# Kernel tuning notes

Hardware: AMD Instinct MI355X
Metric: run time of the kernel (lower is better)

## Reference

```python
import jax, jax.numpy as jnp
import numpy as np

N_NODES = 100000
N_EDGES = 800000
D_MODEL = 128
N_HEAD = 8
LN_EPS = 1e-6


def setup_inputs() -> dict:
    key = jax.random.key(0)
    ks = jax.random.split(key, 6)
    embeds = jax.random.normal(ks[0], (N_NODES, D_MODEL), dtype=jnp.float32)
    # xavier_uniform bound for square [d, d] matrix: sqrt(6 / (d + d))
    bound = float(np.sqrt(6.0 / (D_MODEL + D_MODEL)))
    qW = jax.random.uniform(ks[1], (D_MODEL, D_MODEL), minval=-bound, maxval=bound, dtype=jnp.float32)
    kW = jax.random.uniform(ks[2], (D_MODEL, D_MODEL), minval=-bound, maxval=bound, dtype=jnp.float32)
    vW = jax.random.uniform(ks[3], (D_MODEL, D_MODEL), minval=-bound, maxval=bound, dtype=jnp.float32)
    ln_gamma = jnp.ones((D_MODEL,), dtype=jnp.float32)
    ln_beta = jnp.zeros((D_MODEL,), dtype=jnp.float32)
    edge_index = jax.random.randint(ks[4], (2, N_EDGES), 0, N_NODES, dtype=jnp.int64)
    return {"embeds": embeds, "qW": qW, "kW": kW, "vW": vW,
            "ln_gamma": ln_gamma, "ln_beta": ln_beta, "edge_index": edge_index}


def reference(embeds, qW, kW, vW, ln_gamma, ln_beta, edge_index):
    rows = edge_index[0]  # destination (softmax segment) indices, [E]
    cols = edge_index[1]  # source indices, [E]
    n_nodes, d_model = embeds.shape
    n_edges = rows.shape[0]
    head = N_HEAD
    d_head = d_model // head

    row_e = embeds[rows]                      # [E, d]
    col_e = embeds[cols]                      # [E, d]
    q = (row_e @ qW).reshape(n_edges, head, d_head)
    k = (col_e @ kW).reshape(n_edges, head, d_head)
    v = (col_e @ vW).reshape(n_edges, head, d_head)

    att = jnp.einsum('ehd,ehd->eh', q, k)     # [E, h]
    att = jnp.clip(att, -10.0, 10.0)
    exp_att = jnp.exp(att)

    # segment-softmax normalization over destination node
    att_norm = jax.ops.segment_sum(exp_att, rows, num_segments=n_nodes)  # [N, h]
    att = exp_att / (att_norm[rows] + 1e-8)   # [E, h]

    res_e = (att[:, :, None] * v).reshape(n_edges, d_model)              # [E, d]
    res = jax.ops.segment_sum(res_e, rows, num_segments=n_nodes)         # [N, d]
    res = res + embeds

    # LayerNorm(eps=1e-6) over last dim
    mean = jnp.mean(res, axis=-1, keepdims=True)
    var = jnp.mean((res - mean) ** 2, axis=-1, keepdims=True)
    out = (res - mean) * jax.lax.rsqrt(var + LN_EPS) * ln_gamma + ln_beta
    return out
```

## Files before the change

kernel.cpp:

```cpp
#include <hip/hip_runtime.h>
#include <hip/hip_bf16.h>

#define N_NODES 100000
#define N_EDGES 800000
#define D 128
#define NH 8
#define NB ((N_NODES + 255) / 256)

typedef __hip_bfloat16 bf16;
typedef __bf16 bf16x8 __attribute__((ext_vector_type(8)));
typedef float  f32x4  __attribute__((ext_vector_type(4)));

__device__ __forceinline__ unsigned short f2bu(float x) {
    bf16 b = __float2bfloat16(x);
    return *reinterpret_cast<unsigned short*>(&b);
}
__device__ __forceinline__ float bu2f(unsigned short u) {
    return __uint_as_float(((unsigned)u) << 16);
}
__device__ __forceinline__ float bfe0(unsigned u) { return __uint_as_float(u << 16); }
__device__ __forceinline__ float bfe1(unsigned u) { return __uint_as_float(u & 0xffff0000u); }

union frag_u { unsigned short u[8]; bf16x8 v; };

__global__ __launch_bounds__(256) void wf_prep(
    const float* __restrict__ Wq, const float* __restrict__ Wk, const float* __restrict__ Wv,
    unsigned short* __restrict__ Wf)
{
    int t = blockIdx.x * 256 + threadIdx.x;
    if (t >= 3 * 32 * 64) return;
    int lane = t & 63;
    int ct   = (t >> 6) & 31;
    int mat  = t >> 11;
    const float* W = (mat == 0) ? Wq : (mat == 1) ? Wk : Wv;
    int c  = ct >> 3, tt = ct & 7;
    int n  = tt * 16 + (lane & 15);
    int kb = c * 32 + (lane >> 4) * 8;
    unsigned short* dst = Wf + (size_t)mat * 32768 + (size_t)ct * 1024 + (size_t)lane * 8;
#pragma unroll
    for (int j = 0; j < 8; ++j) {
        float w  = W[(size_t)(kb + j) * D + n];
        unsigned short hb = f2bu(w);
        float lo = w - bu2f(hb);
        dst[j]       = hb;
        dst[512 + j] = f2bu(lo);
    }
}

__global__ __launch_bounds__(256) void qkv_mfma(
    const float* __restrict__ E, const unsigned short* __restrict__ Wf,
    bf16* __restrict__ Q, bf16* __restrict__ K, bf16* __restrict__ V)
{
    __shared__ unsigned short bsh[16384];
    const int tid  = threadIdx.x;
    const int wave = tid >> 6;
    const int lane = tid & 63;
    const int r0w  = blockIdx.x * 128 + wave * 32;

    const int am = lane & 15;
    const int aq = lane >> 4;

    frag_u ahi[2][4], alo[2][4];
#pragma unroll
    for (int rt = 0; rt < 2; ++rt) {
        int row = r0w + rt * 16 + am;
        if (row >= N_NODES) row = N_NODES - 1;
        const float* erow = E + (size_t)row * D + aq * 8;
#pragma unroll
        for (int c = 0; c < 4; ++c) {
            float4 e0 = *reinterpret_cast<const float4*>(erow + c * 32);
            float4 e1 = *reinterpret_cast<const float4*>(erow + c * 32 + 4);
            float ef[8] = {e0.x, e0.y, e0.z, e0.w, e1.x, e1.y, e1.z, e1.w};
#pragma unroll
            for (int j = 0; j < 8; ++j) {
                unsigned short hb = f2bu(ef[j]);
                ahi[rt][c].u[j] = hb;
                alo[rt][c].u[j] = f2bu(ef[j] - bu2f(hb));
            }
        }
    }

    bf16* const Os[3] = {Q, K, V};

#pragma unroll
    for (int mat = 0; mat < 3; ++mat) {
        f32x4 acc[8][2];
#pragma unroll
        for (int t = 0; t < 8; ++t)
#pragma unroll
            for (int rt = 0; rt < 2; ++rt)
                acc[t][rt] = (f32x4){0.f, 0.f, 0.f, 0.f};

        const unsigned short* wm = Wf + (size_t)mat * 32768;

#pragma unroll
        for (int half = 0; half < 2; ++half) {
            __syncthreads();
            const uint4* src = reinterpret_cast<const uint4*>(wm + half * 16384);
            uint4* dstv = reinterpret_cast<uint4*>(bsh);
#pragma unroll
            for (int k = 0; k < 8; ++k)
                dstv[k * 256 + tid] = src[k * 256 + tid];
            __syncthreads();

#pragma unroll
            for (int t = 0; t < 8; ++t) {
#pragma unroll
                for (int cc = 0; cc < 2; ++cc) {
                    const unsigned short* bp = bsh + (cc * 8 + t) * 1024 + lane * 8;
                    bf16x8 bhi = *reinterpret_cast<const bf16x8*>(bp);
                    bf16x8 blo = *reinterpret_cast<const bf16x8*>(bp + 512);
                    const int c = half * 2 + cc;
#pragma unroll
                    for (int rt = 0; rt < 2; ++rt) {
                        acc[t][rt] = __builtin_amdgcn_mfma_f32_16x16x32_bf16(alo[rt][c].v, bhi, acc[t][rt], 0, 0, 0);
                        acc[t][rt] = __builtin_amdgcn_mfma_f32_16x16x32_bf16(ahi[rt][c].v, blo, acc[t][rt], 0, 0, 0);
                        acc[t][rt] = __builtin_amdgcn_mfma_f32_16x16x32_bf16(ahi[rt][c].v, bhi, acc[t][rt], 0, 0, 0);
                    }
                }
            }
        }
        __syncthreads();

        unsigned short* ob = bsh + wave * 2176;
#pragma unroll
        for (int rt = 0; rt < 2; ++rt) {
#pragma unroll
            for (int t = 0; t < 8; ++t)
#pragma unroll
                for (int r = 0; r < 4; ++r)
                    ob[(aq * 4 + r) * 136 + t * 16 + am] = f2bu(acc[t][rt][r]);
            const int row = lane >> 2, c4 = lane & 3;
            int grow = r0w + rt * 16 + row;
            if (grow < N_NODES) {
                const uint4* srcb = reinterpret_cast<const uint4*>(ob + row * 136 + c4 * 32);
                uint4 d0 = srcb[0], d1 = srcb[1], d2 = srcb[2], d3 = srcb[3];
                uint4* dst = reinterpret_cast<uint4*>(Os[mat] + (size_t)grow * D + c4 * 32);
                dst[0] = d0; dst[1] = d1; dst[2] = d2; dst[3] = d3;
            }
        }
    }
}

__global__ __launch_bounds__(256) void hist_kernel(
    const int* __restrict__ rows, int* __restrict__ counts)
{
    int e = blockIdx.x * 256 + threadIdx.x;
    if (e < N_EDGES) atomicAdd(&counts[rows[e]], 1);
}

__global__ __launch_bounds__(256) void scan_block(
    const int* __restrict__ counts, int* __restrict__ scanned, int* __restrict__ block_sums)
{
    __shared__ int s[256];
    int tid = threadIdx.x;
    int i = blockIdx.x * 256 + tid;
    int v = (i < N_NODES) ? counts[i] : 0;
    s[tid] = v;
    __syncthreads();
#pragma unroll
    for (int off = 1; off < 256; off <<= 1) {
        int t = (tid >= off) ? s[tid - off] : 0;
        __syncthreads();
        s[tid] += t;
        __syncthreads();
    }
    if (i < N_NODES) scanned[i] = s[tid] - v;
    if (tid == 255) block_sums[blockIdx.x] = s[255];
}

__global__ __launch_bounds__(512) void scan_tops(int* __restrict__ block_sums)
{
    __shared__ int s[512];
    int tid = threadIdx.x;
    int v = (tid < NB) ? block_sums[tid] : 0;
    s[tid] = v;
    __syncthreads();
#pragma unroll
    for (int off = 1; off < 512; off <<= 1) {
        int t = (tid >= off) ? s[tid - off] : 0;
        __syncthreads();
        s[tid] += t;
        __syncthreads();
    }
    if (tid < NB) block_sums[tid] = s[tid] - v;
}

__global__ __launch_bounds__(256) void scan_add(
    int* __restrict__ scanned, const int* __restrict__ block_sums, int* __restrict__ cursor)
{
    int i = blockIdx.x * 256 + threadIdx.x;
    if (i < N_NODES) {
        int o = scanned[i] + block_sums[blockIdx.x];
        scanned[i] = o;
        cursor[i]  = o;
    }
}

__global__ __launch_bounds__(256) void scatter_kernel(
    const int* __restrict__ rows, const int* __restrict__ cols,
    int* __restrict__ cursor, int* __restrict__ csr_cols)
{
    int e = blockIdx.x * 256 + threadIdx.x;
    if (e < N_EDGES) {
        int pos = atomicAdd(&cursor[rows[e]], 1);
        csr_cols[pos] = cols[e];
    }
}

__global__ __launch_bounds__(256) void fused_node(
    const bf16* __restrict__ Qb, const bf16* __restrict__ Kb, const bf16* __restrict__ Vb,
    const int* __restrict__ offsets, const int* __restrict__ counts,
    const int* __restrict__ csr_cols,
    const float* __restrict__ emb,
    const float* __restrict__ gamma, const float* __restrict__ beta,
    float* __restrict__ out)
{
    int n = blockIdx.x * 4 + (threadIdx.x >> 6);
    int lane = threadIdx.x & 63;
    if (n >= N_NODES) return;

    unsigned qu = *reinterpret_cast<const unsigned*>(Qb + (size_t)n * D + lane * 2);
    float q0 = bfe0(qu), q1 = bfe1(qu);

    int start = offsets[n];
    int cnt   = counts[n];

    const bf16* kbase = Kb + lane * 2;
    const bf16* vbase = Vb + lane * 2;

    float acc0 = 0.f, acc1 = 0.f, nrm = 0.f;
    for (int base = 0; base < cnt; base += 64) {
        int m = cnt - base; if (m > 64) m = 64;
        int myc = (base + lane < cnt) ? csr_cols[start + base + lane] : 0;
        int j = 0;
        for (; j + 1 < m; j += 2) {
            int c0 = __shfl(myc, j, 64);
            int c1 = __shfl(myc, j + 1, 64);
            unsigned ku0 = *reinterpret_cast<const unsigned*>(kbase + (size_t)c0 * D);
            unsigned vu0 = *reinterpret_cast<const unsigned*>(vbase + (size_t)c0 * D);
            unsigned ku1 = *reinterpret_cast<const unsigned*>(kbase + (size_t)c1 * D);
            unsigned vu1 = *reinterpret_cast<const unsigned*>(vbase + (size_t)c1 * D);
            float p0 = q0 * bfe0(ku0) + q1 * bfe1(ku0);
            float p1 = q0 * bfe0(ku1) + q1 * bfe1(ku1);
            p0 += __shfl_xor(p0, 1, 64);
            p1 += __shfl_xor(p1, 1, 64);
            p0 += __shfl_xor(p0, 2, 64);
            p1 += __shfl_xor(p1, 2, 64);
            p0 += __shfl_xor(p0, 4, 64);
            p1 += __shfl_xor(p1, 4, 64);
            float s0 = __expf(fminf(fmaxf(p0, -10.f), 10.f));
            float s1 = __expf(fminf(fmaxf(p1, -10.f), 10.f));
            nrm  += s0 + s1;
            acc0 += s0 * bfe0(vu0) + s1 * bfe0(vu1);
            acc1 += s0 * bfe1(vu0) + s1 * bfe1(vu1);
        }
        if (j < m) {
            int c0 = __shfl(myc, j, 64);
            unsigned ku0 = *reinterpret_cast<const unsigned*>(kbase + (size_t)c0 * D);
            unsigned vu0 = *reinterpret_cast<const unsigned*>(vbase + (size_t)c0 * D);
            float p0 = q0 * bfe0(ku0) + q1 * bfe1(ku0);
            p0 += __shfl_xor(p0, 1, 64);
            p0 += __shfl_xor(p0, 2, 64);
            p0 += __shfl_xor(p0, 4, 64);
            float s0 = __expf(fminf(fmaxf(p0, -10.f), 10.f));
            nrm  += s0;
            acc0 += s0 * bfe0(vu0);
            acc1 += s0 * bfe1(vu0);
        }
    }

    float w = 1.f / (nrm + 1e-8f);
    float2 e2 = *reinterpret_cast<const float2*>(emb + (size_t)n * D + lane * 2);
    float x0 = acc0 * w + e2.x;
    float x1 = acc1 * w + e2.y;

    float ssum = x0 + x1;
#pragma unroll
    for (int off = 32; off; off >>= 1) ssum += __shfl_xor(ssum, off, 64);
    float mean = ssum * (1.0f / 128.0f);
    float d0 = x0 - mean, d1 = x1 - mean;
    float var = d0 * d0 + d1 * d1;
#pragma unroll
    for (int off = 32; off; off >>= 1) var += __shfl_xor(var, off, 64);
    float rs = rsqrtf(var * (1.0f / 128.0f) + 1e-6f);

    float2 g2 = *reinterpret_cast<const float2*>(gamma + lane * 2);
    float2 b2 = *reinterpret_cast<const float2*>(beta + lane * 2);
    float2 o2 = make_float2(d0 * rs * g2.x + b2.x, d1 * rs * g2.y + b2.y);
    *reinterpret_cast<float2*>(out + (size_t)n * D + lane * 2) = o2;
}

extern "C" void kernel_launch(void* const* d_in, const int* in_sizes, int n_in,
                              void* d_out, int out_size, void* d_ws, size_t ws_size,
                              hipStream_t stream)
{
    const float* emb   = (const float*)d_in[0];
    const float* qW    = (const float*)d_in[1];
    const float* kW    = (const float*)d_in[2];
    const float* vW    = (const float*)d_in[3];
    const float* gamma = (const float*)d_in[4];
    const float* beta  = (const float*)d_in[5];
    const int*   eidx  = (const int*)d_in[6];
    const int*   rows  = eidx;
    const int*   cols  = eidx + N_EDGES;
    float* out = (float*)d_out;

    const size_t ND = (size_t)N_NODES * D;
    bf16* Qb = (bf16*)d_ws;
    bf16* Kb = Qb + ND;
    bf16* Vb = Kb + ND;
    int* counts     = (int*)(Vb + ND);
    int* offsets    = counts + N_NODES;
    int* cursor     = offsets + N_NODES;
    int* block_sums = cursor + N_NODES;
    int* csr_cols   = block_sums + 512;
    unsigned short* Wf = (unsigned short*)(csr_cols + N_EDGES);

    hipMemsetAsync(counts, 0, (size_t)N_NODES * sizeof(int), stream);

    wf_prep<<<24, 256, 0, stream>>>(qW, kW, vW, Wf);
    qkv_mfma<<<(N_NODES + 127) / 128, 256, 0, stream>>>(emb, Wf, Qb, Kb, Vb);

    hist_kernel<<<(N_EDGES + 255) / 256, 256, 0, stream>>>(rows, counts);
    scan_block<<<NB, 256, 0, stream>>>(counts, offsets, block_sums);
    scan_tops<<<1, 512, 0, stream>>>(block_sums);
    scan_add<<<NB, 256, 0, stream>>>(offsets, block_sums, cursor);
    scatter_kernel<<<(N_EDGES + 255) / 256, 256, 0, stream>>>(rows, cols, cursor, csr_cols);

    fused_node<<<(N_NODES + 3) / 4, 256, 0, stream>>>(
        Qb, Kb, Vb, offsets, counts, csr_cols, emb, gamma, beta, out);
}
```

Baseline: 315.3 us.

## Interleave K/V per node and process eight edges per wave with per-lane head slices

K and V projections are written into one interleaved [N,256] buffer so each gathered neighbor's K and V sit in one contiguous 512-byte row. The aggregation kernel now assigns each lane a (head, edge-slot) pair, so a wave handles eight edges at once, with each lane loading 32-byte K and V slices and computing a full head dot product locally instead of using shuffle reductions. Partial sums across slots are combined with a shuffle reduction at the end. This trades per-edge shuffles and narrow 4-byte gathers for wider loads and more registers (16 accumulators plus K/V floats), and wastes lanes when a node has a degree not divisible by eight.

```diff
diff --git a/kernel.cpp b/kernel.cpp
--- a/kernel.cpp
+++ b/kernel.cpp
@@ -20,6 +20,13 @@
 }
 __device__ __forceinline__ float bfe0(unsigned u) { return __uint_as_float(u << 16); }
 __device__ __forceinline__ float bfe1(unsigned u) { return __uint_as_float(u & 0xffff0000u); }
+
+__device__ __forceinline__ void ext8(uint4 u, float* f) {
+    f[0] = bfe0(u.x); f[1] = bfe1(u.x);
+    f[2] = bfe0(u.y); f[3] = bfe1(u.y);
+    f[4] = bfe0(u.z); f[5] = bfe1(u.z);
+    f[6] = bfe0(u.w); f[7] = bfe1(u.w);
+}
 
 union frag_u { unsigned short u[8]; bf16x8 v; };
 
@@ -49,7 +56,7 @@
 
 __global__ __launch_bounds__(256) void qkv_mfma(
     const float* __restrict__ E, const unsigned short* __restrict__ Wf,
-    bf16* __restrict__ Q, bf16* __restrict__ K, bf16* __restrict__ V)
+    bf16* __restrict__ Q, bf16* __restrict__ KV)
 {
     __shared__ unsigned short bsh[16384];
     const int tid  = threadIdx.x;
@@ -79,8 +86,6 @@
             }
         }
     }
-
-    bf16* const Os[3] = {Q, K, V};
 
 #pragma unroll
     for (int mat = 0; mat < 3; ++mat) {
@@ -135,7 +140,10 @@
             if (grow < N_NODES) {
                 const uint4* srcb = reinterpret_cast<const uint4*>(ob + row * 136 + c4 * 32);
                 uint4 d0 = srcb[0], d1 = srcb[1], d2 = srcb[2], d3 = srcb[3];
-                uint4* dst = reinterpret_cast<uint4*>(Os[mat] + (size_t)grow * D + c4 * 32);
+                bf16* base = (mat == 0)
+                    ? (Q  + (size_t)grow * D)
+                    : (KV + (size_t)grow * 256 + (mat == 1 ? 0 : 128));
+                uint4* dst = reinterpret_cast<uint4*>(base + c4 * 32);
                 dst[0] = d0; dst[1] = d1; dst[2] = d2; dst[3] = d3;
             }
         }
@@ -209,7 +217,7 @@
 }
 
 __global__ __launch_bounds__(256) void fused_node(
-    const bf16* __restrict__ Qb, const bf16* __restrict__ Kb, const bf16* __restrict__ Vb,
+    const bf16* __restrict__ Qb, const bf16* __restrict__ KV,
     const int* __restrict__ offsets, const int* __restrict__ counts,
     const int* __restrict__ csr_cols,
     const float* __restrict__ emb,
@@ -219,61 +227,62 @@
     int n = blockIdx.x * 4 + (threadIdx.x >> 6);
     int lane = threadIdx.x & 63;
     if (n >= N_NODES) return;
-
-    unsigned qu = *reinterpret_cast<const unsigned*>(Qb + (size_t)n * D + lane * 2);
-    float q0 = bfe0(qu), q1 = bfe1(qu);
+    const int head = lane & 7;
+    const int slot = lane >> 3;
+
+    const uint4* qp = reinterpret_cast<const uint4*>(Qb + (size_t)n * D + head * 16);
+    uint4 qa = qp[0], qb_ = qp[1];
+    float qf[16];
+    ext8(qa, qf); ext8(qb_, qf + 8);
 
     int start = offsets[n];
     int cnt   = counts[n];
 
-    const bf16* kbase = Kb + lane * 2;
-    const bf16* vbase = Vb + lane * 2;
-
-    float acc0 = 0.f, acc1 = 0.f, nrm = 0.f;
+    float acc[16];
+#pragma unroll
+    for (int i = 0; i < 16; ++i) acc[i] = 0.f;
+    float nrm = 0.f;
+
     for (int base = 0; base < cnt; base += 64) {
         int m = cnt - base; if (m > 64) m = 64;
         int myc = (base + lane < cnt) ? csr_cols[start + base + lane] : 0;
-        int j = 0;
-        for (; j + 1 < m; j += 2) {
-            int c0 = __shfl(myc, j, 64);
-            int c1 = __shfl(myc, j + 1, 64);
-            unsigned ku0 = *reinterpret_cast<const unsigned*>(kbase + (size_t)c0 * D);
-            unsigned vu0 = *reinterpret_cast<const unsigned*>(vbase + (size_t)c0 * D);
-            unsigned ku1 = *reinterpret_cast<const unsigned*>(kbase + (size_t)c1 * D);
-            unsigned vu1 = *reinterpret_cast<const unsigned*>(vbase + (size_t)c1 * D);
-            float p0 = q0 * bfe0(ku0) + q1 * bfe1(ku0);
-            float p1 = q0 * bfe0(ku1) + q1 * bfe1(ku1);
-            p0 += __shfl_xor(p0, 1, 64);
-            p1 += __shfl_xor(p1, 1, 64);
-            p0 += __shfl_xor(p0, 2, 64);
-            p1 += __shfl_xor(p1, 2, 64);
-            p0 += __shfl_xor(p0, 4, 64);
-            p1 += __shfl_xor(p1, 4, 64);
-            float s0 = __expf(fminf(fmaxf(p0, -10.f), 10.f));
-            float s1 = __expf(fminf(fmaxf(p1, -10.f), 10.f));
-            nrm  += s0 + s1;
-            acc0 += s0 * bfe0(vu0) + s1 * bfe0(vu1);
-            acc1 += s0 * bfe1(vu0) + s1 * bfe1(vu1);
+        for (int g = 0; g < m; g += 8) {
+            int j = g + slot;
+            int c = __shfl(myc, j, 64);
+            const uint4* kvp = reinterpret_cast<const uint4*>(KV + (size_t)c * 256 + head * 16);
+            uint4 k0 = kvp[0], k1 = kvp[1];
+            uint4 v0 = kvp[16], v1 = kvp[17];
+            float kf[16], vf[16];
+            ext8(k0, kf); ext8(k1, kf + 8);
+            float p = 0.f;
+#pragma unroll
+            for (int i = 0; i < 16; ++i) p += qf[i] * kf[i];
+            float s = __expf(fminf(fmaxf(p, -10.f), 10.f));
+            if (j >= m) s = 0.f;
+            nrm += s;
+            ext8(v0, vf); ext8(v1, vf + 8);
+#pragma unroll
+            for (int i = 0; i < 16; ++i) acc[i] += s * vf[i];
         }
-        if (j < m) {
-            int c0 = __shfl(myc, j, 64);
-            unsigned ku0 = *reinterpret_cast<const unsigned*>(kbase + (size_t)c0 * D);
-            unsigned vu0 = *reinterpret_cast<const unsigned*>(vbase + (size_t)c0 * D);
-            float p0 = q0 * bfe0(ku0) + q1 * bfe1(ku0);
-            p0 += __shfl_xor(p0, 1, 64);
-            p0 += __shfl_xor(p0, 2, 64);
-            p0 += __shfl_xor(p0, 4, 64);
-            float s0 = __expf(fminf(fmaxf(p0, -10.f), 10.f));
-            nrm  += s0;
-            acc0 += s0 * bfe0(vu0);
-            acc1 += s0 * bfe1(vu0);
-        }
+    }
+
+#pragma unroll
+    for (int off = 8; off <= 32; off <<= 1) {
+        nrm += __shfl_xor(nrm, off, 64);
+#pragma unroll
+        for (int i = 0; i < 16; ++i) acc[i] += __shfl_xor(acc[i], off, 64);
     }
 
     float w = 1.f / (nrm + 1e-8f);
-    float2 e2 = *reinterpret_cast<const float2*>(emb + (size_t)n * D + lane * 2);
-    float x0 = acc0 * w + e2.x;
-    float x1 = acc1 * w + e2.y;
+    float a0 = 0.f, a1 = 0.f;
+#pragma unroll
+    for (int s2 = 0; s2 < 8; ++s2)
+        if (slot == s2) { a0 = acc[2 * s2]; a1 = acc[2 * s2 + 1]; }
+
+    int di = head * 16 + slot * 2;
+    float2 e2 = *reinterpret_cast<const float2*>(emb + (size_t)n * D + di);
+    float x0 = a0 * w + e2.x;
+    float x1 = a1 * w + e2.y;
 
     float ssum = x0 + x1;
 #pragma unroll
@@ -285,10 +294,10 @@
     for (int off = 32; off; off >>= 1) var += __shfl_xor(var, off, 64);
     float rs = rsqrtf(var * (1.0f / 128.0f) + 1e-6f);
 
-    float2 g2 = *reinterpret_cast<const float2*>(gamma + lane * 2);
-    float2 b2 = *reinterpret_cast<const float2*>(beta + lane * 2);
+    float2 g2 = *reinterpret_cast<const float2*>(gamma + di);
+    float2 b2 = *reinterpret_cast<const float2*>(beta + di);
     float2 o2 = make_float2(d0 * rs * g2.x + b2.x, d1 * rs * g2.y + b2.y);
-    *reinterpret_cast<float2*>(out + (size_t)n * D + lane * 2) = o2;
+    *reinterpret_cast<float2*>(out + (size_t)n * D + di) = o2;
 }
 
 extern "C" void kernel_launch(void* const* d_in, const int* in_sizes, int n_in,
@@ -308,9 +317,8 @@
 
     const size_t ND = (size_t)N_NODES * D;
     bf16* Qb = (bf16*)d_ws;
-    bf16* Kb = Qb + ND;
-    bf16* Vb = Kb + ND;
-    int* counts     = (int*)(Vb + ND);
+    bf16* KV = Qb + ND;
+    int* counts     = (int*)(KV + 2 * ND);
     int* offsets    = counts + N_NODES;
     int* cursor     = offsets + N_NODES;
     int* block_sums = cursor + N_NODES;
@@ -320,7 +328,7 @@
     hipMemsetAsync(counts, 0, (size_t)N_NODES * sizeof(int), stream);
 
     wf_prep<<<24, 256, 0, stream>>>(qW, kW, vW, Wf);
-    qkv_mfma<<<(N_NODES + 127) / 128, 256, 0, stream>>>(emb, Wf, Qb, Kb, Vb);
+    qkv_mfma<<<(N_NODES + 127) / 128, 256, 0, stream>>>(emb, Wf, Qb, KV);
 
     hist_kernel<<<(N_EDGES + 255) / 256, 256, 0, stream>>>(rows, counts);
     scan_block<<<NB, 256, 0, stream>>>(counts, offsets, block_sums);
@@ -329,5 +337,5 @@
     scatter_kernel<<<(N_EDGES + 255) / 256, 256, 0, stream>>>(rows, cols, cursor, csr_cols);
 
     fused_node<<<(N_NODES + 3) / 4, 256, 0, stream>>>(
-        Qb, Kb, Vb, offsets, counts, csr_cols, emb, gamma, beta, out);
-}
+        Qb, KV, offsets, counts, csr_cols, emb, gamma, beta, out);
+}
```

New measurement: 324.3 us. 2.9% more time.

## Fuse CSR build into one persistent kernel with software grid barriers

Applied to the files above, without the earlier changes.

Replaces the histogram, three-stage scan and scatter kernels with a single csr_build kernel of NB (391) blocks. The stages are separated by atomic-counter grid barriers, and blocks spin with s_sleep while they wait. The memset of counts and barriers is folded into the weight-prep kernel. The aim is to cut launch overhead and inter-kernel gaps, four launches plus a memset. The barrier assumes all 391 blocks are co-resident, which should hold on MI355X, and the spinning blocks add atomic traffic.

```diff
diff --git a/kernel.cpp b/kernel.cpp
--- a/kernel.cpp
+++ b/kernel.cpp
@@ -23,27 +23,30 @@
 
 union frag_u { unsigned short u[8]; bf16x8 v; };
 
-__global__ __launch_bounds__(256) void wf_prep(
+__global__ __launch_bounds__(256) void prep_zero(
     const float* __restrict__ Wq, const float* __restrict__ Wk, const float* __restrict__ Wv,
-    unsigned short* __restrict__ Wf)
+    unsigned short* __restrict__ Wf, int* __restrict__ counts, int* __restrict__ bars)
 {
     int t = blockIdx.x * 256 + threadIdx.x;
-    if (t >= 3 * 32 * 64) return;
-    int lane = t & 63;
-    int ct   = (t >> 6) & 31;
-    int mat  = t >> 11;
-    const float* W = (mat == 0) ? Wq : (mat == 1) ? Wk : Wv;
-    int c  = ct >> 3, tt = ct & 7;
-    int n  = tt * 16 + (lane & 15);
-    int kb = c * 32 + (lane >> 4) * 8;
-    unsigned short* dst = Wf + (size_t)mat * 32768 + (size_t)ct * 1024 + (size_t)lane * 8;
-#pragma unroll
-    for (int j = 0; j < 8; ++j) {
-        float w  = W[(size_t)(kb + j) * D + n];
-        unsigned short hb = f2bu(w);
-        float lo = w - bu2f(hb);
-        dst[j]       = hb;
-        dst[512 + j] = f2bu(lo);
+    if (t < N_NODES) counts[t] = 0;
+    if (t < 8) bars[t] = 0;
+    if (t < 3 * 32 * 64) {
+        int lane = t & 63;
+        int ct   = (t >> 6) & 31;
+        int mat  = t >> 11;
+        const float* W = (mat == 0) ? Wq : (mat == 1) ? Wk : Wv;
+        int c  = ct >> 3, tt = ct & 7;
+        int n  = tt * 16 + (lane & 15);
+        int kb = c * 32 + (lane >> 4) * 8;
+        unsigned short* dst = Wf + (size_t)mat * 32768 + (size_t)ct * 1024 + (size_t)lane * 8;
+#pragma unroll
+        for (int j = 0; j < 8; ++j) {
+            float w  = W[(size_t)(kb + j) * D + n];
+            unsigned short hb = f2bu(w);
+            float lo = w - bu2f(hb);
+            dst[j]       = hb;
+            dst[512 + j] = f2bu(lo);
+        }
     }
 }
 
@@ -142,67 +145,78 @@
     }
 }
 
-__global__ __launch_bounds__(256) void hist_kernel(
-    const int* __restrict__ rows, int* __restrict__ counts)
-{
-    int e = blockIdx.x * 256 + threadIdx.x;
-    if (e < N_EDGES) atomicAdd(&counts[rows[e]], 1);
-}
-
-__global__ __launch_bounds__(256) void scan_block(
-    const int* __restrict__ counts, int* __restrict__ scanned, int* __restrict__ block_sums)
-{
+__device__ __forceinline__ void gridbar(int* bar) {
+    __syncthreads();
+    if (threadIdx.x == 0) {
+        __hip_atomic_fetch_add(bar, 1, __ATOMIC_ACQ_REL, __HIP_MEMORY_SCOPE_AGENT);
+        while (__hip_atomic_load(bar, __ATOMIC_ACQUIRE, __HIP_MEMORY_SCOPE_AGENT) < NB)
+            __builtin_amdgcn_s_sleep(2);
+    }
+    __syncthreads();
+}
+
+__global__ __launch_bounds__(256) void csr_build(
+    const int* __restrict__ rows, const int* __restrict__ cols,
+    int* __restrict__ counts, int* __restrict__ offsets, int* __restrict__ cursor,
+    int* __restrict__ block_sums, int* __restrict__ block_pref,
+    int* __restrict__ csr_cols, int* __restrict__ bars)
+{
+    const int tid = threadIdx.x;
+    const int b   = blockIdx.x;
+    const int gt  = b * 256 + tid;
     __shared__ int s[256];
-    int tid = threadIdx.x;
-    int i = blockIdx.x * 256 + tid;
-    int v = (i < N_NODES) ? counts[i] : 0;
+    __shared__ int s2[256];
+    __shared__ int bpref_sh;
+
+    for (int e = gt; e < N_EDGES; e += NB * 256)
+        atomicAdd(&counts[rows[e]], 1);
+    gridbar(&bars[0]);
+
+    int v = (gt < N_NODES)
+        ? __hip_atomic_load(&counts[gt], __ATOMIC_RELAXED, __HIP_MEMORY_SCOPE_AGENT)
+        : 0;
     s[tid] = v;
     __syncthreads();
 #pragma unroll
     for (int off = 1; off < 256; off <<= 1) {
-        int t = (tid >= off) ? s[tid - off] : 0;
+        int t2 = (tid >= off) ? s[tid - off] : 0;
         __syncthreads();
-        s[tid] += t;
+        s[tid] += t2;
         __syncthreads();
     }
-    if (i < N_NODES) scanned[i] = s[tid] - v;
-    if (tid == 255) block_sums[blockIdx.x] = s[255];
-}
-
-__global__ __launch_bounds__(512) void scan_tops(int* __restrict__ block_sums)
-{
-    __shared__ int s[512];
-    int tid = threadIdx.x;
-    int v = (tid < NB) ? block_sums[tid] : 0;
-    s[tid] = v;
+    int excl = s[tid] - v;
+    if (tid == 255) block_sums[b] = s[255];
+    gridbar(&bars[1]);
+
+    if (b == 0) {
+        int va = (tid < NB)
+            ? __hip_atomic_load(&block_sums[tid], __ATOMIC_RELAXED, __HIP_MEMORY_SCOPE_AGENT) : 0;
+        int vb = (tid + 256 < NB)
+            ? __hip_atomic_load(&block_sums[tid + 256], __ATOMIC_RELAXED, __HIP_MEMORY_SCOPE_AGENT) : 0;
+        s[tid] = va; s2[tid] = vb;
+        __syncthreads();
+#pragma unroll
+        for (int off = 1; off < 256; off <<= 1) {
+            int ta = (tid >= off) ? s[tid - off] : 0;
+            int tb = (tid >= off) ? s2[tid - off] : 0;
+            __syncthreads();
+            s[tid] += ta; s2[tid] += tb;
+            __syncthreads();
+        }
+        int totala = s[255];
+        block_pref[tid] = s[tid] - va;
+        if (tid + 256 < NB) block_pref[tid + 256] = totala + s2[tid] - vb;
+    }
+    gridbar(&bars[2]);
+
+    if (tid == 0)
+        bpref_sh = __hip_atomic_load(&block_pref[b], __ATOMIC_RELAXED, __HIP_MEMORY_SCOPE_AGENT);
     __syncthreads();
-#pragma unroll
-    for (int off = 1; off < 512; off <<= 1) {
-        int t = (tid >= off) ? s[tid - off] : 0;
-        __syncthreads();
-        s[tid] += t;
-        __syncthreads();
-    }
-    if (tid < NB) block_sums[tid] = s[tid] - v;
-}
-
-__global__ __launch_bounds__(256) void scan_add(
-    int* __restrict__ scanned, const int* __restrict__ block_sums, int* __restrict__ cursor)
-{
-    int i = blockIdx.x * 256 + threadIdx.x;
-    if (i < N_NODES) {
-        int o = scanned[i] + block_sums[blockIdx.x];
-        scanned[i] = o;
-        cursor[i]  = o;
-    }
-}
-
-__global__ __launch_bounds__(256) void scatter_kernel(
-    const int* __restrict__ rows, const int* __restrict__ cols,
-    int* __restrict__ cursor, int* __restrict__ csr_cols)
-{
-    int e = blockIdx.x * 256 + threadIdx.x;
-    if (e < N_EDGES) {
+    int o = excl + bpref_sh;
+    if (gt < N_NODES) { offsets[gt] = o; cursor[gt] = o; }
+    gridbar(&bars[3]);
+
+    for (int e = gt; e < N_EDGES; e += NB * 256) {
         int pos = atomicAdd(&cursor[rows[e]], 1);
         csr_cols[pos] = cols[e];
     }
@@ -314,20 +328,15 @@
     int* offsets    = counts + N_NODES;
     int* cursor     = offsets + N_NODES;
     int* block_sums = cursor + N_NODES;
-    int* csr_cols   = block_sums + 512;
+    int* block_pref = block_sums + 512;
+    int* bars       = block_pref + 512;
+    int* csr_cols   = bars + 8;
     unsigned short* Wf = (unsigned short*)(csr_cols + N_EDGES);
 
-    hipMemsetAsync(counts, 0, (size_t)N_NODES * sizeof(int), stream);
-
-    wf_prep<<<24, 256, 0, stream>>>(qW, kW, vW, Wf);
+    prep_zero<<<NB, 256, 0, stream>>>(qW, kW, vW, Wf, counts, bars);
     qkv_mfma<<<(N_NODES + 127) / 128, 256, 0, stream>>>(emb, Wf, Qb, Kb, Vb);
-
-    hist_kernel<<<(N_EDGES + 255) / 256, 256, 0, stream>>>(rows, counts);
-    scan_block<<<NB, 256, 0, stream>>>(counts, offsets, block_sums);
-    scan_tops<<<1, 512, 0, stream>>>(block_sums);
-    scan_add<<<NB, 256, 0, stream>>>(offsets, block_sums, cursor);
-    scatter_kernel<<<(N_EDGES + 255) / 256, 256, 0, stream>>>(rows, cols, cursor, csr_cols);
-
+    csr_build<<<NB, 256, 0, stream>>>(rows, cols, counts, offsets, cursor,
+                                      block_sums, block_pref, csr_cols, bars);
     fused_node<<<(N_NODES + 3) / 4, 256, 0, stream>>>(
         Qb, Kb, Vb, offsets, counts, csr_cols, emb, gamma, beta, out);
 }
```

After: 451.7 us. 43.3% more time.
